# Kernel optimization log

Measured on AMD Instinct MI355X. Metric: run time of the kernel, lower is better.

The kernel has to match this reference:

```python
import jax, jax.numpy as jnp
import numpy as np

B, SQ, SKV = 8, 1, 8192
HIDDEN, NUM_HEADS, NUM_KV_HEADS, HEAD_DIM = 4096, 32, 8, 128


def _rotate_half(x):
    x1, x2 = jnp.split(x, 2, axis=-1)
    return jnp.concatenate([-x2, x1], axis=-1)


def setup_inputs() -> dict:
    key = jax.random.key(0)
    ks = jax.random.split(key, 9)
    f = jnp.float32
    return {
        "hidden_states": jax.random.normal(ks[0], (B, SQ, HIDDEN), f),
        "wq": jax.random.normal(ks[1], (HIDDEN, NUM_HEADS * HEAD_DIM), f) * 0.02,
        "wo": jax.random.normal(ks[2], (NUM_HEADS * HEAD_DIM, HIDDEN), f) * 0.02,
        "cos": jax.random.uniform(ks[3], (B, SQ, HEAD_DIM), f, -1.0, 1.0),
        "sin": jax.random.uniform(ks[4], (B, SQ, HEAD_DIM), f, -1.0, 1.0),
        "key_states": jax.random.normal(ks[5], (B, SQ, NUM_KV_HEADS, HEAD_DIM), f),
        "value_states": jax.random.normal(ks[6], (B, SQ, NUM_KV_HEADS, HEAD_DIM), f),
        "k_cache": jax.random.normal(ks[7], (B, SKV, NUM_KV_HEADS, HEAD_DIM), f),
        "v_cache": jax.random.normal(ks[8], (B, SKV, NUM_KV_HEADS, HEAD_DIM), f),
    }


def reference(hidden_states, wq, wo, cos, sin, key_states, value_states, k_cache, v_cache):
    b, sq, _ = hidden_states.shape
    d = cos.shape[-1]
    nkv = key_states.shape[2]
    nh = wq.shape[1] // d
    g = nh // nkv  # GQA group size

    # Q projection -> [b, sq, nh, d]
    q = (hidden_states @ wq).reshape(b, sq, nh, d)

    # inline RoPE on q and the new k (cos/sin broadcast over heads)
    c = cos[:, :, None, :]
    s = sin[:, :, None, :]
    q = q * c + _rotate_half(q) * s
    k_new = key_states * c + _rotate_half(key_states) * s

    # cache append
    K = jnp.concatenate([k_cache, k_new], axis=1)          # [b, skv+sq, nkv, d]
    V = jnp.concatenate([v_cache, value_states], axis=1)   # [b, skv+sq, nkv, d]

    # GQA attention without materializing repeated KV heads
    qr = q.reshape(b, sq, nkv, g, d)
    scale = d ** -0.5
    scores = jnp.einsum('bqngd,bknd->bngqk', qr, K) * scale  # [b,nkv,g,sq,skv+sq]
    probs = jax.nn.softmax(scores, axis=-1)
    out = jnp.einsum('bngqk,bknd->bqngd', probs, V).reshape(b, sq, nh * d)

    # O projection
    return out @ wo
```

## Files before the change

kernel.cpp:

```cpp
#include <hip/hip_runtime.h>

#define HIDDEN 4096
#define NH 32
#define NKV 8
#define HD 128
#define SKV 8192
#define SPLITS 16
#define NPART 64
#define PSTRIDE 520
#define SCALE 0.08838834764831845f

__device__ __forceinline__ float4 ld4(const float* p){ return *(const float4*)p; }

__global__ __launch_bounds__(256) void gemv_part(const float* __restrict__ vec,
                                                 const float* __restrict__ mat,
                                                 float* __restrict__ part)
{
    const int jb  = blockIdx.x;
    const int c   = blockIdx.y;
    const int tid = threadIdx.x;
    const int j0  = jb*1024 + tid*4;

    __shared__ float hid[64*8];
    {
        int t = tid;
        int b0 = t >> 6, i0 = t & 63;
        hid[i0*8 + b0] = vec[(size_t)b0*HIDDEN + c*64 + i0];
        t += 256;
        int b1 = t >> 6, i1 = t & 63;
        hid[i1*8 + b1] = vec[(size_t)b1*HIDDEN + c*64 + i1];
    }
    __syncthreads();

    float4 acc[8];
#pragma unroll
    for (int b=0;b<8;b++) acc[b] = make_float4(0.f,0.f,0.f,0.f);

    const float* mp = mat + (size_t)c*64*HIDDEN + j0;
#pragma unroll 8
    for (int ii=0; ii<64; ii++) {
        float4 w  = ld4(mp + (size_t)ii*HIDDEN);
        float4 h0 = *(const float4*)&hid[ii*8];
        float4 h1 = *(const float4*)&hid[ii*8+4];
        acc[0].x += h0.x*w.x; acc[0].y += h0.x*w.y; acc[0].z += h0.x*w.z; acc[0].w += h0.x*w.w;
        acc[1].x += h0.y*w.x; acc[1].y += h0.y*w.y; acc[1].z += h0.y*w.z; acc[1].w += h0.y*w.w;
        acc[2].x += h0.z*w.x; acc[2].y += h0.z*w.y; acc[2].z += h0.z*w.z; acc[2].w += h0.z*w.w;
        acc[3].x += h0.w*w.x; acc[3].y += h0.w*w.y; acc[3].z += h0.w*w.z; acc[3].w += h0.w*w.w;
        acc[4].x += h1.x*w.x; acc[4].y += h1.x*w.y; acc[4].z += h1.x*w.z; acc[4].w += h1.x*w.w;
        acc[5].x += h1.y*w.x; acc[5].y += h1.y*w.y; acc[5].z += h1.y*w.z; acc[5].w += h1.y*w.w;
        acc[6].x += h1.z*w.x; acc[6].y += h1.z*w.y; acc[6].z += h1.z*w.z; acc[6].w += h1.z*w.w;
        acc[7].x += h1.w*w.x; acc[7].y += h1.w*w.y; acc[7].z += h1.w*w.z; acc[7].w += h1.w*w.w;
    }
#pragma unroll
    for (int b=0;b<8;b++)
        *(float4*)(part + ((size_t)(c*8+b))*HIDDEN + j0) = acc[b];
}

__global__ __launch_bounds__(256) void q_reduce_rope(const float* __restrict__ part,
                                                     const float* __restrict__ cosb,
                                                     const float* __restrict__ sinb,
                                                     float* __restrict__ q_rope)
{
    const int b    = blockIdx.x >> 5;
    const int jseg = blockIdx.x & 31;
    const int tid  = threadIdx.x;
    const int jl   = tid & 127;
    const int cg   = tid >> 7;

    float a = 0.f;
    const float* pp = part + (size_t)(cg*32*8 + b)*HIDDEN + jseg*128 + jl;
#pragma unroll 8
    for (int c=0;c<32;c++) a += pp[(size_t)c*8*HIDDEN];

    __shared__ float lds[256];
    __shared__ float sum[128];
    lds[tid] = a;
    __syncthreads();
    if (tid < 128) sum[tid] = lds[tid] + lds[tid+128];
    __syncthreads();
    if (tid < 128) {
        const int d = tid;
        float x = sum[d];
        float p = sum[d ^ 64];
        float cv = cosb[b*HD + d], sv = sinb[b*HD + d];
        float r = (d < 64) ? (x*cv - p*sv) : (x*cv + p*sv);
        q_rope[(size_t)b*HIDDEN + jseg*128 + d] = r;
    }
}

__global__ __launch_bounds__(256) void attn_split(const float* __restrict__ qr,
                                                  const float* __restrict__ kc,
                                                  const float* __restrict__ vc,
                                                  float* __restrict__ part)
{
    const int split = blockIdx.x;
    const int n     = blockIdx.y;
    const int b     = blockIdx.z;
    const int tid   = threadIdx.x;
    const int wave  = tid >> 6;
    const int lane  = tid & 63;
    const int kg    = lane >> 4;
    const int dl    = lane & 15;

    float4 q1[4], q2[4];
    const float* qb = qr + ((size_t)b*NH + n*4)*HD;
#pragma unroll
    for (int h=0;h<4;h++){
        float4 x = ld4(qb + h*HD + dl*4);
        float4 y = ld4(qb + h*HD + 64 + dl*4);
        q1[h] = make_float4(x.x*SCALE, x.y*SCALE, x.z*SCALE, x.w*SCALE);
        q2[h] = make_float4(y.x*SCALE, y.y*SCALE, y.z*SCALE, y.w*SCALE);
    }
    float l[4] = {0.f,0.f,0.f,0.f};
    float4 acc1[4], acc2[4];
#pragma unroll
    for (int h=0;h<4;h++){
        acc1[h] = make_float4(0.f,0.f,0.f,0.f);
        acc2[h] = make_float4(0.f,0.f,0.f,0.f);
    }

    const float* kb = kc + ((size_t)b*SKV*NKV + n)*HD;
    const float* vb = vc + ((size_t)b*SKV*NKV + n)*HD;

    int t0 = split*512 + wave*16;
    for (int iter=0; iter<8; iter++, t0 += 64) {
#pragma unroll
        for (int it=0; it<4; it++){
            const int k = t0 + it*4 + kg;
            const float* kp = kb + (size_t)k*(NKV*HD);
            const float* vp = vb + (size_t)k*(NKV*HD);
            float4 k1 = ld4(kp + dl*4);
            float4 k2 = ld4(kp + 64 + dl*4);
            float4 v1 = ld4(vp + dl*4);
            float4 v2 = ld4(vp + 64 + dl*4);
            float p[4];
#pragma unroll
            for (int h=0;h<4;h++){
                float sp = q1[h].x*k1.x + q1[h].y*k1.y + q1[h].z*k1.z + q1[h].w*k1.w
                         + q2[h].x*k2.x + q2[h].y*k2.y + q2[h].z*k2.z + q2[h].w*k2.w;
                sp += __shfl_xor(sp, 1);
                sp += __shfl_xor(sp, 2);
                sp += __shfl_xor(sp, 4);
                sp += __shfl_xor(sp, 8);
                p[h] = __expf(sp);
                l[h] += p[h];
            }
#pragma unroll
            for (int h=0;h<4;h++){
                float ph = p[h];
                acc1[h].x += ph*v1.x; acc1[h].y += ph*v1.y;
                acc1[h].z += ph*v1.z; acc1[h].w += ph*v1.w;
                acc2[h].x += ph*v2.x; acc2[h].y += ph*v2.y;
                acc2[h].z += ph*v2.z; acc2[h].w += ph*v2.w;
            }
        }
    }

#pragma unroll
    for (int h=0;h<4;h++){
        float t;
        t = l[h];      t += __shfl_xor(t,16); t += __shfl_xor(t,32); l[h] = t;
        t = acc1[h].x; t += __shfl_xor(t,16); t += __shfl_xor(t,32); acc1[h].x = t;
        t = acc1[h].y; t += __shfl_xor(t,16); t += __shfl_xor(t,32); acc1[h].y = t;
        t = acc1[h].z; t += __shfl_xor(t,16); t += __shfl_xor(t,32); acc1[h].z = t;
        t = acc1[h].w; t += __shfl_xor(t,16); t += __shfl_xor(t,32); acc1[h].w = t;
        t = acc2[h].x; t += __shfl_xor(t,16); t += __shfl_xor(t,32); acc2[h].x = t;
        t = acc2[h].y; t += __shfl_xor(t,16); t += __shfl_xor(t,32); acc2[h].y = t;
        t = acc2[h].z; t += __shfl_xor(t,16); t += __shfl_xor(t,32); acc2[h].z = t;
        t = acc2[h].w; t += __shfl_xor(t,16); t += __shfl_xor(t,32); acc2[h].w = t;
    }

    float* pb = part + ((size_t)((b*NKV + n)*SPLITS + split)*4 + wave)*PSTRIDE;
    if (lane == 0){
#pragma unroll
        for (int h=0;h<4;h++) pb[h] = l[h];
    }
    if (kg == 0){
#pragma unroll
        for (int h=0;h<4;h++){
            *(float4*)(pb + 8 + h*HD + dl*4)      = acc1[h];
            *(float4*)(pb + 8 + h*HD + 64 + dl*4) = acc2[h];
        }
    }
}

__global__ __launch_bounds__(256) void attn_combine(const float* __restrict__ part,
                                                    const float* __restrict__ qr,
                                                    const float* __restrict__ knew,
                                                    const float* __restrict__ vnew,
                                                    const float* __restrict__ cosb,
                                                    const float* __restrict__ sinb,
                                                    float* __restrict__ attn_out)
{
    const int bn  = blockIdx.x;
    const int b   = bn >> 3;
    const int n   = bn & 7;
    const int tid = threadIdx.x;
    const int wave = tid >> 6;
    const int lane = tid & 63;
    const float* pp = part + (size_t)bn*NPART*PSTRIDE;

    __shared__ float sm[4];
    __shared__ float lds_l[NPART*4];

    lds_l[tid] = pp[(size_t)(tid>>2)*PSTRIDE + (tid&3)];

    {
        const float* kn = knew + (size_t)bn*HD;
        const float* cb = cosb + (size_t)b*HD;
        const float* sb = sinb + (size_t)b*HD;
        const float* qh = qr + ((size_t)b*NH + n*4 + wave)*HD;
        float k_lo = kn[lane], k_hi = kn[lane+64];
        float kr1 = k_lo*cb[lane]    - k_hi*sb[lane];
        float kr2 = k_hi*cb[lane+64] + k_lo*sb[lane+64];
        float sp = (qh[lane]*kr1 + qh[lane+64]*kr2) * SCALE;
        sp += __shfl_xor(sp, 1);
        sp += __shfl_xor(sp, 2);
        sp += __shfl_xor(sp, 4);
        sp += __shfl_xor(sp, 8);
        sp += __shfl_xor(sp, 16);
        sp += __shfl_xor(sp, 32);
        if (lane == 0) sm[wave] = __expf(sp);
    }
    __syncthreads();

    const int o = tid*2;
    const int h = o >> 7;
    const int d = o & 127;
    const float wn = sm[h];
    float L = wn;
#pragma unroll 8
    for (int p=0; p<NPART; p++) L += lds_l[p*4+h];

    const float* vn = vnew + (size_t)bn*HD;
    float a0 = wn * vn[d];
    float a1 = wn * vn[d+1];
    const float* ap = pp + 8 + h*HD + d;
#pragma unroll 8
    for (int p=0; p<NPART; p++){
        float2 v = *(const float2*)(ap + (size_t)p*PSTRIDE);
        a0 += v.x; a1 += v.y;
    }
    const float inv = 1.f / L;
    float* op = attn_out + ((size_t)b*NH + n*4 + h)*HD + d;
    op[0] = a0*inv; op[1] = a1*inv;
}

__global__ __launch_bounds__(256) void o_reduce(const float* __restrict__ part,
                                                float* __restrict__ out)
{
    const int b    = blockIdx.x >> 5;
    const int jseg = blockIdx.x & 31;
    const int tid  = threadIdx.x;
    const int jl   = tid & 127;
    const int cg   = tid >> 7;

    float a = 0.f;
    const float* pp = part + (size_t)(cg*32*8 + b)*HIDDEN + jseg*128 + jl;
#pragma unroll 8
    for (int c=0;c<32;c++) a += pp[(size_t)c*8*HIDDEN];

    __shared__ float lds[256];
    lds[tid] = a;
    __syncthreads();
    if (tid < 128)
        out[(size_t)b*HIDDEN + jseg*128 + tid] = lds[tid] + lds[tid+128];
}

extern "C" void kernel_launch(void* const* d_in, const int* in_sizes, int n_in,
                              void* d_out, int out_size, void* d_ws, size_t ws_size,
                              hipStream_t stream) {
    const float* hidden = (const float*)d_in[0];
    const float* wq     = (const float*)d_in[1];
    const float* wo     = (const float*)d_in[2];
    const float* cosb   = (const float*)d_in[3];
    const float* sinb   = (const float*)d_in[4];
    const float* knew   = (const float*)d_in[5];
    const float* vnew   = (const float*)d_in[6];
    const float* kc     = (const float*)d_in[7];
    const float* vc     = (const float*)d_in[8];
    float* out = (float*)d_out;

    float* ws        = (float*)d_ws;
    float* part      = ws;
    float* q_rope    = ws + 2097152;
    float* attn_out  = q_rope + 32768;
    float* attn_part = attn_out + 32768;

    gemv_part<<<dim3(4,64), 256, 0, stream>>>(hidden, wq, part);
    q_reduce_rope<<<256, 256, 0, stream>>>(part, cosb, sinb, q_rope);
    attn_split<<<dim3(SPLITS, NKV, 8), 256, 0, stream>>>(q_rope, kc, vc, attn_part);
    attn_combine<<<64, 256, 0, stream>>>(attn_part, q_rope, knew, vnew, cosb, sinb, attn_out);
    gemv_part<<<dim3(4,64), 256, 0, stream>>>(attn_out, wo, part);
    o_reduce<<<256, 256, 0, stream>>>(part, out);
}
```

Before: 649.8 us.

## Stream contiguous KV tiles into LDS with double-buffered global_load_lds

The split-attention kernel is reorganised so each 512-thread block covers all 8 KV heads for a 128-key slice, with one wave per KV head. K and V rows are now read as fully contiguous chunks through direct global-to-LDS loads into a double buffer, replacing strided per-head global reads. The goal is better coalescing and overlap of HBM streaming with the dot-product and accumulate work. In exchange there is a block barrier every 4 keys and 64KB of LDS per block, which may limit occupancy and adds a synchronisation-correctness risk for the async LDS loads.

```diff
diff --git a/kernel.cpp b/kernel.cpp
--- a/kernel.cpp
+++ b/kernel.cpp
@@ -5,12 +5,22 @@
 #define NKV 8
 #define HD 128
 #define SKV 8192
-#define SPLITS 16
+#define S2 64
+#define KPB 128
+#define BUF 4
+#define NT (KPB/BUF)
 #define NPART 64
 #define PSTRIDE 520
 #define SCALE 0.08838834764831845f
 
 __device__ __forceinline__ float4 ld4(const float* p){ return *(const float4*)p; }
+
+__device__ __forceinline__ void gll16(const float* g, float* l){
+    __builtin_amdgcn_global_load_lds(
+        (const __attribute__((address_space(1))) unsigned int*)g,
+        (__attribute__((address_space(3))) unsigned int*)l,
+        16, 0, 0);
+}
 
 __global__ __launch_bounds__(256) void gemv_part(const float* __restrict__ vec,
                                                  const float* __restrict__ mat,
@@ -88,22 +98,24 @@
     }
 }
 
-__global__ __launch_bounds__(256) void attn_split(const float* __restrict__ qr,
+__global__ __launch_bounds__(512) void attn_split(const float* __restrict__ qr,
                                                   const float* __restrict__ kc,
                                                   const float* __restrict__ vc,
                                                   float* __restrict__ part)
 {
     const int split = blockIdx.x;
-    const int n     = blockIdx.y;
-    const int b     = blockIdx.z;
+    const int b     = blockIdx.y;
     const int tid   = threadIdx.x;
     const int wave  = tid >> 6;
     const int lane  = tid & 63;
     const int kg    = lane >> 4;
     const int dl    = lane & 15;
 
+    __shared__ __align__(16) float bufK[2][BUF*1024];
+    __shared__ __align__(16) float bufV[2][BUF*1024];
+
     float4 q1[4], q2[4];
-    const float* qb = qr + ((size_t)b*NH + n*4)*HD;
+    const float* qb = qr + ((size_t)b*NH + wave*4)*HD;
 #pragma unroll
     for (int h=0;h<4;h++){
         float4 x = ld4(qb + h*HD + dl*4);
@@ -111,6 +123,7 @@
         q1[h] = make_float4(x.x*SCALE, x.y*SCALE, x.z*SCALE, x.w*SCALE);
         q2[h] = make_float4(y.x*SCALE, y.y*SCALE, y.z*SCALE, y.w*SCALE);
     }
+
     float l[4] = {0.f,0.f,0.f,0.f};
     float4 acc1[4], acc2[4];
 #pragma unroll
@@ -119,20 +132,40 @@
         acc2[h] = make_float4(0.f,0.f,0.f,0.f);
     }
 
-    const float* kb = kc + ((size_t)b*SKV*NKV + n)*HD;
-    const float* vb = vc + ((size_t)b*SKV*NKV + n)*HD;
-
-    int t0 = split*512 + wave*16;
-    for (int iter=0; iter<8; iter++, t0 += 64) {
-#pragma unroll
-        for (int it=0; it<4; it++){
-            const int k = t0 + it*4 + kg;
-            const float* kp = kb + (size_t)k*(NKV*HD);
-            const float* vp = vb + (size_t)k*(NKV*HD);
-            float4 k1 = ld4(kp + dl*4);
-            float4 k2 = ld4(kp + 64 + dl*4);
-            float4 v1 = ld4(vp + dl*4);
-            float4 v2 = ld4(vp + 64 + dl*4);
+    const float* kbase = kc + ((size_t)b*SKV + (size_t)split*KPB)*(NKV*HD);
+    const float* vbase = vc + ((size_t)b*SKV + (size_t)split*KPB)*(NKV*HD);
+
+    const int woff = wave*256 + lane*4;
+
+    {
+        const float* gk = kbase;
+        const float* gv = vbase;
+        gll16(gk + woff,        &bufK[0][wave*256]);
+        gll16(gk + 2048 + woff, &bufK[0][2048 + wave*256]);
+        gll16(gv + woff,        &bufV[0][wave*256]);
+        gll16(gv + 2048 + woff, &bufV[0][2048 + wave*256]);
+    }
+    __syncthreads();
+
+    int cur = 0;
+    for (int t = 0; t < NT; ++t) {
+        if (t + 1 < NT) {
+            const float* gk = kbase + (size_t)(t+1)*(BUF*1024);
+            const float* gv = vbase + (size_t)(t+1)*(BUF*1024);
+            const int nb = cur ^ 1;
+            gll16(gk + woff,        &bufK[nb][wave*256]);
+            gll16(gk + 2048 + woff, &bufK[nb][2048 + wave*256]);
+            gll16(gv + woff,        &bufV[nb][wave*256]);
+            gll16(gv + 2048 + woff, &bufV[nb][2048 + wave*256]);
+        }
+
+        {
+            const float* Kb = &bufK[cur][kg*1024 + wave*128];
+            const float* Vb = &bufV[cur][kg*1024 + wave*128];
+            float4 k1 = ld4(Kb + dl*4);
+            float4 k2 = ld4(Kb + 64 + dl*4);
+            float4 v1 = ld4(Vb + dl*4);
+            float4 v2 = ld4(Vb + 64 + dl*4);
             float p[4];
 #pragma unroll
             for (int h=0;h<4;h++){
@@ -154,6 +187,9 @@
                 acc2[h].z += ph*v2.z; acc2[h].w += ph*v2.w;
             }
         }
+
+        __syncthreads();
+        cur ^= 1;
     }
 
 #pragma unroll
@@ -170,7 +206,7 @@
         t = acc2[h].w; t += __shfl_xor(t,16); t += __shfl_xor(t,32); acc2[h].w = t;
     }
 
-    float* pb = part + ((size_t)((b*NKV + n)*SPLITS + split)*4 + wave)*PSTRIDE;
+    float* pb = part + ((size_t)((b*NKV + wave)*S2 + split))*PSTRIDE;
     if (lane == 0){
 #pragma unroll
         for (int h=0;h<4;h++) pb[h] = l[h];
@@ -289,7 +325,7 @@
 
     gemv_part<<<dim3(4,64), 256, 0, stream>>>(hidden, wq, part);
     q_reduce_rope<<<256, 256, 0, stream>>>(part, cosb, sinb, q_rope);
-    attn_split<<<dim3(SPLITS, NKV, 8), 256, 0, stream>>>(q_rope, kc, vc, attn_part);
+    attn_split<<<dim3(S2, 8), 512, 0, stream>>>(q_rope, kc, vc, attn_part);
     attn_combine<<<64, 256, 0, stream>>>(attn_part, q_rope, knew, vnew, cosb, sinb, attn_out);
     gemv_part<<<dim3(4,64), 256, 0, stream>>>(attn_out, wo, part);
     o_reduce<<<256, 256, 0, stream>>>(part, out);
```

Result: faster. 631.5 us (-2.8%).
